# Kernel optimization log

Hardware: AMD Instinct MI355X
Metric: run time of the kernel (lower is better)

Reference implementation:

```python
import jax, jax.numpy as jnp
import numpy as np

B, C, O, H, W, K = 8, 64, 64, 96, 96, 3
PAD = 1


def setup_inputs() -> dict:
    key = jax.random.key(0)
    ks = jax.random.split(key, 5)
    x = jax.random.normal(ks[0], (B, C, H, W), jnp.float32)
    # small offset weights so sampled offsets stay O(1) pixel, like a trained net
    offset_w = jax.random.normal(ks[1], (2 * K * K, C, K, K), jnp.float32) * 0.01
    offset_b = jnp.zeros((2 * K * K,), jnp.float32)
    conv_w = jax.random.normal(ks[2], (O, C, K, K), jnp.float32) * (1.0 / np.sqrt(C * K * K))
    conv_b = jax.random.normal(ks[3], (O,), jnp.float32) * 0.01
    return {"x": x, "offset_w": offset_w, "offset_b": offset_b,
            "conv_w": conv_w, "conv_b": conv_b}


def _conv2d(x, w, b, pad):
    out = jax.lax.conv_general_dilated(
        x, w, window_strides=(1, 1), padding=[(pad, pad), (pad, pad)],
        dimension_numbers=("NCHW", "OIHW", "NCHW"))
    return out + b[None, :, None, None]


def _gather(x_flat, yi, xi):
    # x_flat: [B, C, H*W]; yi, xi: [B, K2, H, W] int32 sample indices
    valid = (yi >= 0) & (yi < H) & (xi >= 0) & (xi < W)
    idx = jnp.clip(yi, 0, H - 1) * W + jnp.clip(xi, 0, W - 1)
    idx_f = idx.reshape(idx.shape[0], -1)  # [B, K2*H*W]
    vals = jax.vmap(lambda xf, i: xf[:, i])(x_flat, idx_f)  # [B, C, K2*H*W]
    vals = vals.reshape(x_flat.shape[0], x_flat.shape[1], *idx.shape[1:])
    return vals * valid[:, None].astype(vals.dtype)  # zero padding outside


def _deform_conv2d(x, offset, w, b, pad):
    # Faithful to torchvision.ops.deform_conv2d (v1, 1 offset group, stride 1)
    K2 = K * K
    off = offset.reshape(offset.shape[0], K2, 2, H, W)
    dy, dx = off[:, :, 0], off[:, :, 1]  # (dy, dx) per kernel tap, torchvision order
    ky = jnp.repeat(jnp.arange(K), K).astype(x.dtype)  # row index i of tap k=i*K+j
    kx = jnp.tile(jnp.arange(K), K).astype(x.dtype)    # col index j
    # fractional sample positions [B, K2, H, W]
    py = jnp.arange(H, dtype=x.dtype)[None, None, :, None] - pad + ky[None, :, None, None] + dy
    px = jnp.arange(W, dtype=x.dtype)[None, None, None, :] - pad + kx[None, :, None, None] + dx
    y0 = jnp.floor(py)
    x0 = jnp.floor(px)
    wy = (py - y0)[:, None]  # broadcast over channels
    wx = (px - x0)[:, None]
    y0i = y0.astype(jnp.int32)
    x0i = x0.astype(jnp.int32)
    x_flat = x.reshape(x.shape[0], x.shape[1], H * W)
    g00 = _gather(x_flat, y0i, x0i)
    g01 = _gather(x_flat, y0i, x0i + 1)
    g10 = _gather(x_flat, y0i + 1, x0i)
    g11 = _gather(x_flat, y0i + 1, x0i + 1)
    # bilinear interp -> sampled patches [B, C, K2, H, W]
    sampled = (g00 * (1 - wy) * (1 - wx) + g01 * (1 - wy) * wx
               + g10 * wy * (1 - wx) + g11 * wy * wx)
    out = jnp.einsum("bckhw,ock->bohw", sampled, w.reshape(w.shape[0], w.shape[1], K2))
    return out + b[None, :, None, None]


def reference(x, offset_w, offset_b, conv_w, conv_b):
    offset = _conv2d(x, offset_w, offset_b, PAD)  # [B, 18, H, W]
    return _deform_conv2d(x, offset, conv_w, conv_b, PAD)
```

## Files before the change

kernel.cpp:

```cpp
#include <hip/hip_runtime.h>

#define Bb 8
#define Cc 64
#define Oo 64
#define Hh 96
#define Ww 96
#define HW 9216
#define NOFF 18

typedef __bf16 bf16_t;
typedef __bf16 bf16x2 __attribute__((ext_vector_type(2)));
typedef __bf16 bf16x8 __attribute__((ext_vector_type(8)));
typedef float  f32x4  __attribute__((ext_vector_type(4)));

#define XT_SZ   (Bb*HW*Cc)
#define WTPD_SZ (18*4*64*8)
#define WTPO_SZ (18*2*64*8)

__global__ void xpose_prep(const float* __restrict__ x, const float* __restrict__ cw,
                           const float* __restrict__ ow, bf16_t* __restrict__ xt,
                           bf16_t* __restrict__ wtpd, bf16_t* __restrict__ wtpo) {
    __shared__ float tile[64][65];
    int bid = blockIdx.x;
    if (bid < 1152) {
        int b    = bid / 144;
        int t0   = (bid % 144) * 64;
        int lane = threadIdx.x & 63;
        int sub  = threadIdx.x >> 6;
        const float* xb = x + (size_t)b * Cc * HW;
        #pragma unroll
        for (int i = 0; i < 16; ++i) {
            int c = sub * 16 + i;
            tile[c][lane] = xb[c * HW + t0 + lane];
        }
        __syncthreads();
        bf16_t* xtb = xt + ((size_t)b * HW + t0) * Cc;
        int half = lane >> 5, cpair = lane & 31;
        #pragma unroll
        for (int i = 0; i < 8; ++i) {
            int hw = sub * 16 + half * 8 + i;
            bf16x2 v;
            v[0] = (bf16_t)tile[cpair * 2][hw];
            v[1] = (bf16_t)tile[cpair * 2 + 1][hw];
            *(bf16x2*)&xtb[hw * Cc + cpair * 2] = v;
        }
    } else if (bid < 1170) {
        int n = (bid - 1152) * 256 + threadIdx.x;
        int t = n >> 8; int rem = n & 255; int mt = rem >> 6; int l = rem & 63;
        int o = mt * 16 + (l & 15);
        int kbase = t * 32 + ((l >> 4) & 3) * 8;
        bf16x8 v;
        #pragma unroll
        for (int j = 0; j < 8; ++j) {
            int kidx = kbase + j; int k = kidx >> 6; int c = kidx & 63;
            v[j] = (bf16_t)cw[(o * 64 + c) * 9 + k];
        }
        *(bf16x8*)&wtpd[n * 8] = v;
    } else {
        int n = (bid - 1170) * 256 + threadIdx.x;
        int t = n >> 7; int rem = n & 127; int mt = rem >> 6; int l = rem & 63;
        int oc = mt * 16 + (l & 15);
        int kbase = t * 32 + ((l >> 4) & 3) * 8;
        bf16x8 v;
        #pragma unroll
        for (int j = 0; j < 8; ++j) {
            int kidx = kbase + j; int k = kidx >> 6; int c = kidx & 63;
            v[j] = (oc < NOFF) ? (bf16_t)ow[(oc * 64 + c) * 9 + k] : (bf16_t)0.f;
        }
        *(bf16x8*)&wtpo[n * 8] = v;
    }
}

__global__ __launch_bounds__(256, 3) void fused_dcn(const bf16_t* __restrict__ xt,
        const bf16_t* __restrict__ wtpo, const bf16_t* __restrict__ wtpd,
        const float* __restrict__ ob, const float* __restrict__ cb,
        float* __restrict__ out) {
    __shared__ float offbuf[64 * 20];
    __shared__ bf16_t Sa[4][16 * 72];
    __shared__ bf16_t slab[16 * 16 * Cc];

    int bid = blockIdx.x;
    int b = bid & 7;
    int t8 = bid >> 3;
    int h0 = (t8 / 12) * 8, w0 = (t8 % 12) * 8;
    int tid = threadIdx.x, lane = tid & 63, q = tid >> 6;
    int cg = lane & 7, prow = lane >> 3;
    int cb8 = cg * 8;
    bf16_t* myS = &Sa[q][0];
    int bbase = b * HW;

    int wy0 = min(max(h0 - 4, 0), Hh - 16);
    int wx0 = min(max(w0 - 4, 0), Ww - 16);

    {
        bf16x8 st[8];
        #pragma unroll
        for (int i = 0; i < 8; ++i) {
            int seg = q * 8 + i;
            int row = seg >> 1, half = seg & 1;
            const bf16_t* src = xt + (size_t)(bbase + (wy0 + row) * Ww + wx0) * Cc
                              + half * 512 + lane * 8;
            st[i] = *(const bf16x8*)src;
        }
        #pragma unroll
        for (int i = 0; i < 8; ++i) {
            int seg = q * 8 + i;
            *(bf16x8*)&slab[seg * 512 + lane * 8] = st[i];
        }
    }

    int pl[2], ph[2], pw[2];
    #pragma unroll
    for (int i = 0; i < 2; ++i) {
        pl[i] = q * 16 + i * 8 + prow;
        ph[i] = h0 + q * 2 + i;
        pw[i] = w0 + prow;
    }

    const bf16x8* wtpo_v = (const bf16x8*)wtpo;
    const bf16x8* wtpd_v = (const bf16x8*)wtpd;

    {
        f32x4 acc[2];
        #pragma unroll
        for (int mt = 0; mt < 2; ++mt)
            #pragma unroll
            for (int r = 0; r < 4; ++r) {
                int oc = mt * 16 + ((lane >> 4) & 3) * 4 + r;
                acc[mt][r] = (oc < NOFF) ? ob[oc] : 0.f;
            }
        bf16x8 g[2];
        bf16x8 wreg[2][2][2];
        auto issue = [&](int k, bf16x8 (&gg)[2]) {
            const int ky = k / 3, kx = k % 3;
            #pragma unroll
            for (int i = 0; i < 2; ++i) {
                int y = ph[i] - 1 + ky, x = pw[i] - 1 + kx;
                bool valid = (y >= 0) && (y < Hh) && (x >= 0) && (x < Ww);
                bf16x8 v;
                #pragma unroll
                for (int j = 0; j < 8; ++j) v[j] = (bf16_t)0.f;
                if (valid)
                    v = *(const bf16x8*)&slab[((y - wy0) * 16 + (x - wx0)) * Cc + cb8];
                gg[i] = v;
            }
        };
        auto loadw = [&](int k, bf16x8 (&w)[2][2]) {
            #pragma unroll
            for (int s = 0; s < 2; ++s)
                #pragma unroll
                for (int mt = 0; mt < 2; ++mt)
                    w[s][mt] = wtpo_v[((k * 2 + s) * 2 + mt) * 64 + lane];
        };
        loadw(0, wreg[0]);
        __syncthreads();
        issue(0, g);
        #pragma unroll
        for (int k = 0; k < 9; ++k) {
            #pragma unroll
            for (int i = 0; i < 2; ++i)
                *(bf16x8*)&myS[(i * 8 + prow) * 72 + cb8] = g[i];
            if (k < 8) { issue(k + 1, g); loadw(k + 1, wreg[(k + 1) & 1]); }
            #pragma unroll
            for (int s = 0; s < 2; ++s) {
                bf16x8 bfrag = *(bf16x8*)&myS[(lane & 15) * 72 + s * 32 + ((lane >> 4) & 3) * 8];
                #pragma unroll
                for (int mt = 0; mt < 2; ++mt)
                    acc[mt] = __builtin_amdgcn_mfma_f32_16x16x32_bf16(wreg[k & 1][s][mt], bfrag, acc[mt], 0, 0, 0);
            }
        }
        #pragma unroll
        for (int mt = 0; mt < 2; ++mt)
            #pragma unroll
            for (int r = 0; r < 4; ++r) {
                int oc = mt * 16 + ((lane >> 4) & 3) * 4 + r;
                if (oc < NOFF)
                    offbuf[(q * 16 + (lane & 15)) * 20 + oc] = acc[mt][r];
            }
    }

    f32x4 acc[4];
    #pragma unroll
    for (int mt = 0; mt < 4; ++mt)
        #pragma unroll
        for (int r = 0; r < 4; ++r)
            acc[mt][r] = cb[mt * 16 + ((lane >> 4) & 3) * 4 + r];

    bf16x8 g[2][4];
    float w4[2][4];
    bf16x8 wreg[2][2][4];
    auto issue = [&](int k, bf16x8 (&gg)[2][4], float (&ww)[2][4]) {
        const int ky = k / 3, kx = k % 3;
        #pragma unroll
        for (int i = 0; i < 2; ++i) {
            float2 od = *(float2*)&offbuf[pl[i] * 20 + 2 * k];
            float py = (float)(ph[i] - 1 + ky) + od.x;
            float px = (float)(pw[i] - 1 + kx) + od.y;
            float fy = floorf(py), fx = floorf(px);
            float wy = py - fy, wx = px - fx;
            int y0 = (int)fy, x0 = (int)fx;
            int y1 = y0 + 1, x1 = x0 + 1;
            bool vy0 = (unsigned)y0 < (unsigned)Hh, vy1 = (unsigned)y1 < (unsigned)Hh;
            bool vx0 = (unsigned)x0 < (unsigned)Ww, vx1 = (unsigned)x1 < (unsigned)Ww;
            ww[i][0] = (vy0 && vx0) ? (1.f - wy) * (1.f - wx) : 0.f;
            ww[i][1] = (vy0 && vx1) ? (1.f - wy) * wx : 0.f;
            ww[i][2] = (vy1 && vx0) ? wy * (1.f - wx) : 0.f;
            ww[i][3] = (vy1 && vx1) ? wy * wx : 0.f;
            int sy0 = min(max(y0 - wy0, 0), 15), sy1 = min(max(y1 - wy0, 0), 15);
            int sx0 = min(max(x0 - wx0, 0), 15), sx1 = min(max(x1 - wx0, 0), 15);
            const bf16_t* r0 = &slab[sy0 * (16 * Cc) + cb8];
            const bf16_t* r1 = &slab[sy1 * (16 * Cc) + cb8];
            gg[i][0] = *(const bf16x8*)(r0 + sx0 * Cc);
            gg[i][1] = *(const bf16x8*)(r0 + sx1 * Cc);
            gg[i][2] = *(const bf16x8*)(r1 + sx0 * Cc);
            gg[i][3] = *(const bf16x8*)(r1 + sx1 * Cc);
        }
    };
    auto loadw = [&](int k, bf16x8 (&w)[2][4]) {
        #pragma unroll
        for (int s = 0; s < 2; ++s)
            #pragma unroll
            for (int mt = 0; mt < 4; ++mt)
                w[s][mt] = wtpd_v[((k * 2 + s) * 4 + mt) * 64 + lane];
    };
    issue(0, g, w4);
    loadw(0, wreg[0]);
    #pragma unroll
    for (int k = 0; k < 9; ++k) {
        #pragma unroll
        for (int i = 0; i < 2; ++i) {
            bf16x8 v;
            #pragma unroll
            for (int j = 0; j < 8; ++j) {
                float s = (float)g[i][0][j] * w4[i][0] + (float)g[i][1][j] * w4[i][1]
                        + (float)g[i][2][j] * w4[i][2] + (float)g[i][3][j] * w4[i][3];
                v[j] = (bf16_t)s;
            }
            *(bf16x8*)&myS[(i * 8 + prow) * 72 + cb8] = v;
        }
        if (k < 8) { issue(k + 1, g, w4); loadw(k + 1, wreg[(k + 1) & 1]); }
        #pragma unroll
        for (int s = 0; s < 2; ++s) {
            bf16x8 bfrag = *(bf16x8*)&myS[(lane & 15) * 72 + s * 32 + ((lane >> 4) & 3) * 8];
            #pragma unroll
            for (int mt = 0; mt < 4; ++mt)
                acc[mt] = __builtin_amdgcn_mfma_f32_16x16x32_bf16(wreg[k & 1][s][mt], bfrag, acc[mt], 0, 0, 0);
        }
    }
    #pragma unroll
    for (int mt = 0; mt < 4; ++mt)
        #pragma unroll
        for (int r = 0; r < 4; ++r) {
            int o = mt * 16 + ((lane >> 4) & 3) * 4 + r;
            int pix = q * 16 + (lane & 15);
            out[(b * Oo + o) * HW + (h0 + (pix >> 3)) * Ww + w0 + (pix & 7)] = acc[mt][r];
        }
}

extern "C" void kernel_launch(void* const* d_in, const int* in_sizes, int n_in,
                              void* d_out, int out_size, void* d_ws, size_t ws_size,
                              hipStream_t stream) {
    const float* x  = (const float*)d_in[0];
    const float* ow = (const float*)d_in[1];
    const float* ob = (const float*)d_in[2];
    const float* cw = (const float*)d_in[3];
    const float* cb = (const float*)d_in[4];
    float* out = (float*)d_out;

    bf16_t* xt   = (bf16_t*)d_ws;
    bf16_t* wtpd = xt + XT_SZ;
    bf16_t* wtpo = wtpd + WTPD_SZ;

    xpose_prep<<<1179, 256, 0, stream>>>(x, cw, ow, xt, wtpd, wtpo);
    fused_dcn <<<1152, 256, 0, stream>>>(xt, wtpo, wtpd, ob, cb, out);
}
```

Baseline: 107.1 us.

## Apply bilinear weights after MFMA on raw corner samples read directly from swizzled slab

The deform stage no longer blends four corners into a bf16 tile per tap. It now runs separate MFMAs on each of the four raw corner samples, read straight from an XOR-swizzled LDS slab, and scales the fp32 results by per-pixel bilinear weights. This drops the per-warp staging buffer, the LDS write/read round trip and the fp32 blend ALU work, and avoids the extra bf16 rounding of the blended value. In exchange it does four times as many MFMAs in the deform stage and adds scalar FMA accumulation, and it removes the software prefetch of weights and samples. The prep kernel's block-to-batch mapping is also interleaved.

```diff
diff --git a/kernel.cpp b/kernel.cpp
--- a/kernel.cpp
+++ b/kernel.cpp
@@ -23,8 +23,8 @@
     __shared__ float tile[64][65];
     int bid = blockIdx.x;
     if (bid < 1152) {
-        int b    = bid / 144;
-        int t0   = (bid % 144) * 64;
+        int b    = bid & 7;
+        int t0   = (bid >> 3) * 64;
         int lane = threadIdx.x & 63;
         int sub  = threadIdx.x >> 6;
         const float* xb = x + (size_t)b * Cc * HW;
@@ -76,7 +76,6 @@
         const float* __restrict__ ob, const float* __restrict__ cb,
         float* __restrict__ out) {
     __shared__ float offbuf[64 * 20];
-    __shared__ bf16_t Sa[4][16 * 72];
     __shared__ bf16_t slab[16 * 16 * Cc];
 
     int bid = blockIdx.x;
@@ -84,9 +83,6 @@
     int t8 = bid >> 3;
     int h0 = (t8 / 12) * 8, w0 = (t8 % 12) * 8;
     int tid = threadIdx.x, lane = tid & 63, q = tid >> 6;
-    int cg = lane & 7, prow = lane >> 3;
-    int cb8 = cg * 8;
-    bf16_t* myS = &Sa[q][0];
     int bbase = b * HW;
 
     int wy0 = min(max(h0 - 4, 0), Hh - 16);
@@ -102,157 +98,132 @@
                               + half * 512 + lane * 8;
             st[i] = *(const bf16x8*)src;
         }
-        #pragma unroll
-        for (int i = 0; i < 8; ++i) {
-            int seg = q * 8 + i;
-            *(bf16x8*)&slab[seg * 512 + lane * 8] = st[i];
-        }
-    }
-
-    int pl[2], ph[2], pw[2];
-    #pragma unroll
-    for (int i = 0; i < 2; ++i) {
-        pl[i] = q * 16 + i * 8 + prow;
-        ph[i] = h0 + q * 2 + i;
-        pw[i] = w0 + prow;
-    }
+        int swz = ((lane >> 3) << 6) + (((lane & 7) ^ ((lane >> 3) & 7)) << 3);
+        #pragma unroll
+        for (int i = 0; i < 8; ++i)
+            *(bf16x8*)&slab[(q * 8 + i) * 512 + swz] = st[i];
+    }
+
+    int g4 = (lane >> 4) & 3;
+    int p  = lane & 15;
+    int py_i = h0 + q * 2 + (p >> 3);
+    int px_i = w0 + (p & 7);
 
     const bf16x8* wtpo_v = (const bf16x8*)wtpo;
     const bf16x8* wtpd_v = (const bf16x8*)wtpd;
 
+    bf16x8 bz;
+    #pragma unroll
+    for (int j = 0; j < 8; ++j) bz[j] = (bf16_t)0.f;
+
+    __syncthreads();
+
     {
         f32x4 acc[2];
         #pragma unroll
         for (int mt = 0; mt < 2; ++mt)
             #pragma unroll
             for (int r = 0; r < 4; ++r) {
-                int oc = mt * 16 + ((lane >> 4) & 3) * 4 + r;
+                int oc = mt * 16 + g4 * 4 + r;
                 acc[mt][r] = (oc < NOFF) ? ob[oc] : 0.f;
             }
-        bf16x8 g[2];
-        bf16x8 wreg[2][2][2];
-        auto issue = [&](int k, bf16x8 (&gg)[2]) {
+        #pragma unroll
+        for (int k = 0; k < 9; ++k) {
             const int ky = k / 3, kx = k % 3;
-            #pragma unroll
-            for (int i = 0; i < 2; ++i) {
-                int y = ph[i] - 1 + ky, x = pw[i] - 1 + kx;
-                bool valid = (y >= 0) && (y < Hh) && (x >= 0) && (x < Ww);
-                bf16x8 v;
+            int y = py_i - 1 + ky, x = px_i - 1 + kx;
+            bool valid = ((unsigned)y < (unsigned)Hh) && ((unsigned)x < (unsigned)Ww);
+            int pl = (y - wy0) * 16 + (x - wx0);
+            pl = min(max(pl, 0), 255);
+            int idx0 = pl * 64 + ((g4 ^ (pl & 7)) << 3);
+            bf16x8 b0 = *(const bf16x8*)&slab[idx0];
+            bf16x8 b1 = *(const bf16x8*)&slab[idx0 ^ 32];
+            if (!valid) { b0 = bz; b1 = bz; }
+            #pragma unroll
+            for (int mt = 0; mt < 2; ++mt) {
+                bf16x8 w0f = wtpo_v[((k * 2 + 0) * 2 + mt) * 64 + lane];
+                acc[mt] = __builtin_amdgcn_mfma_f32_16x16x32_bf16(w0f, b0, acc[mt], 0, 0, 0);
+            }
+            #pragma unroll
+            for (int mt = 0; mt < 2; ++mt) {
+                bf16x8 w1f = wtpo_v[((k * 2 + 1) * 2 + mt) * 64 + lane];
+                acc[mt] = __builtin_amdgcn_mfma_f32_16x16x32_bf16(w1f, b1, acc[mt], 0, 0, 0);
+            }
+        }
+        #pragma unroll
+        for (int mt = 0; mt < 2; ++mt)
+            #pragma unroll
+            for (int r = 0; r < 4; ++r) {
+                int oc = mt * 16 + g4 * 4 + r;
+                if (oc < NOFF)
+                    offbuf[(q * 16 + p) * 20 + oc] = acc[mt][r];
+            }
+    }
+
+    f32x4 acc[4];
+    #pragma unroll
+    for (int mt = 0; mt < 4; ++mt)
+        #pragma unroll
+        for (int r = 0; r < 4; ++r)
+            acc[mt][r] = cb[mt * 16 + g4 * 4 + r];
+
+    const f32x4 z = {0.f, 0.f, 0.f, 0.f};
+    float fyb = (float)(py_i - 1);
+    float fxb = (float)(px_i - 1);
+
+    #pragma unroll
+    for (int k = 0; k < 9; ++k) {
+        const int ky = k / 3, kx = k % 3;
+        float2 od = *(float2*)&offbuf[(q * 16 + p) * 20 + 2 * k];
+        float py = fyb + (float)ky + od.x;
+        float px = fxb + (float)kx + od.y;
+        float fy = floorf(py), fx = floorf(px);
+        float wy = py - fy, wx = px - fx;
+        int y0 = (int)fy, x0 = (int)fx;
+        int y1 = y0 + 1, x1 = x0 + 1;
+        bool vy0 = (unsigned)y0 < (unsigned)Hh, vy1 = (unsigned)y1 < (unsigned)Hh;
+        bool vx0 = (unsigned)x0 < (unsigned)Ww, vx1 = (unsigned)x1 < (unsigned)Ww;
+        float wy1 = 1.f - wy, wx1 = 1.f - wx;
+        float wc[4];
+        wc[0] = (vy0 && vx0) ? wy1 * wx1 : 0.f;
+        wc[1] = (vy0 && vx1) ? wy1 * wx  : 0.f;
+        wc[2] = (vy1 && vx0) ? wy  * wx1 : 0.f;
+        wc[3] = (vy1 && vx1) ? wy  * wx  : 0.f;
+        int pl00 = (y0 - wy0) * 16 + (x0 - wx0);
+        int pls[4];
+        pls[0] = min(max(pl00,      0), 255);
+        pls[1] = min(max(pl00 +  1, 0), 255);
+        pls[2] = min(max(pl00 + 16, 0), 255);
+        pls[3] = min(max(pl00 + 17, 0), 255);
+
+        bf16x8 wf[2][4];
+        #pragma unroll
+        for (int s = 0; s < 2; ++s)
+            #pragma unroll
+            for (int mt = 0; mt < 4; ++mt)
+                wf[s][mt] = wtpd_v[((k * 2 + s) * 4 + mt) * 64 + lane];
+
+        #pragma unroll
+        for (int c = 0; c < 4; ++c) {
+            int idx0 = pls[c] * 64 + ((g4 ^ (pls[c] & 7)) << 3);
+            bf16x8 b0 = *(const bf16x8*)&slab[idx0];
+            bf16x8 b1 = *(const bf16x8*)&slab[idx0 ^ 32];
+            #pragma unroll
+            for (int mt = 0; mt < 4; ++mt) {
+                f32x4 t = __builtin_amdgcn_mfma_f32_16x16x32_bf16(wf[0][mt], b0, z, 0, 0, 0);
+                t = __builtin_amdgcn_mfma_f32_16x16x32_bf16(wf[1][mt], b1, t, 0, 0, 0);
                 #pragma unroll
-                for (int j = 0; j < 8; ++j) v[j] = (bf16_t)0.f;
-                if (valid)
-                    v = *(const bf16x8*)&slab[((y - wy0) * 16 + (x - wx0)) * Cc + cb8];
-                gg[i] = v;
-            }
-        };
-        auto loadw = [&](int k, bf16x8 (&w)[2][2]) {
-            #pragma unroll
-            for (int s = 0; s < 2; ++s)
-                #pragma unroll
-                for (int mt = 0; mt < 2; ++mt)
-                    w[s][mt] = wtpo_v[((k * 2 + s) * 2 + mt) * 64 + lane];
-        };
-        loadw(0, wreg[0]);
-        __syncthreads();
-        issue(0, g);
-        #pragma unroll
-        for (int k = 0; k < 9; ++k) {
-            #pragma unroll
-            for (int i = 0; i < 2; ++i)
-                *(bf16x8*)&myS[(i * 8 + prow) * 72 + cb8] = g[i];
-            if (k < 8) { issue(k + 1, g); loadw(k + 1, wreg[(k + 1) & 1]); }
-            #pragma unroll
-            for (int s = 0; s < 2; ++s) {
-                bf16x8 bfrag = *(bf16x8*)&myS[(lane & 15) * 72 + s * 32 + ((lane >> 4) & 3) * 8];
-                #pragma unroll
-                for (int mt = 0; mt < 2; ++mt)
-                    acc[mt] = __builtin_amdgcn_mfma_f32_16x16x32_bf16(wreg[k & 1][s][mt], bfrag, acc[mt], 0, 0, 0);
-            }
-        }
-        #pragma unroll
-        for (int mt = 0; mt < 2; ++mt)
-            #pragma unroll
-            for (int r = 0; r < 4; ++r) {
-                int oc = mt * 16 + ((lane >> 4) & 3) * 4 + r;
-                if (oc < NOFF)
-                    offbuf[(q * 16 + (lane & 15)) * 20 + oc] = acc[mt][r];
-            }
-    }
-
-    f32x4 acc[4];
+                for (int r = 0; r < 4; ++r)
+                    acc[mt][r] += wc[c] * t[r];
+            }
+        }
+    }
+
     #pragma unroll
     for (int mt = 0; mt < 4; ++mt)
         #pragma unroll
-        for (int r = 0; r < 4; ++r)
-            acc[mt][r] = cb[mt * 16 + ((lane >> 4) & 3) * 4 + r];
-
-    bf16x8 g[2][4];
-    float w4[2][4];
-    bf16x8 wreg[2][2][4];
-    auto issue = [&](int k, bf16x8 (&gg)[2][4], float (&ww)[2][4]) {
-        const int ky = k / 3, kx = k % 3;
-        #pragma unroll
-        for (int i = 0; i < 2; ++i) {
-            float2 od = *(float2*)&offbuf[pl[i] * 20 + 2 * k];
-            float py = (float)(ph[i] - 1 + ky) + od.x;
-            float px = (float)(pw[i] - 1 + kx) + od.y;
-            float fy = floorf(py), fx = floorf(px);
-            float wy = py - fy, wx = px - fx;
-            int y0 = (int)fy, x0 = (int)fx;
-            int y1 = y0 + 1, x1 = x0 + 1;
-            bool vy0 = (unsigned)y0 < (unsigned)Hh, vy1 = (unsigned)y1 < (unsigned)Hh;
-            bool vx0 = (unsigned)x0 < (unsigned)Ww, vx1 = (unsigned)x1 < (unsigned)Ww;
-            ww[i][0] = (vy0 && vx0) ? (1.f - wy) * (1.f - wx) : 0.f;
-            ww[i][1] = (vy0 && vx1) ? (1.f - wy) * wx : 0.f;
-            ww[i][2] = (vy1 && vx0) ? wy * (1.f - wx) : 0.f;
-            ww[i][3] = (vy1 && vx1) ? wy * wx : 0.f;
-            int sy0 = min(max(y0 - wy0, 0), 15), sy1 = min(max(y1 - wy0, 0), 15);
-            int sx0 = min(max(x0 - wx0, 0), 15), sx1 = min(max(x1 - wx0, 0), 15);
-            const bf16_t* r0 = &slab[sy0 * (16 * Cc) + cb8];
-            const bf16_t* r1 = &slab[sy1 * (16 * Cc) + cb8];
-            gg[i][0] = *(const bf16x8*)(r0 + sx0 * Cc);
-            gg[i][1] = *(const bf16x8*)(r0 + sx1 * Cc);
-            gg[i][2] = *(const bf16x8*)(r1 + sx0 * Cc);
-            gg[i][3] = *(const bf16x8*)(r1 + sx1 * Cc);
-        }
-    };
-    auto loadw = [&](int k, bf16x8 (&w)[2][4]) {
-        #pragma unroll
-        for (int s = 0; s < 2; ++s)
-            #pragma unroll
-            for (int mt = 0; mt < 4; ++mt)
-                w[s][mt] = wtpd_v[((k * 2 + s) * 4 + mt) * 64 + lane];
-    };
-    issue(0, g, w4);
-    loadw(0, wreg[0]);
-    #pragma unroll
-    for (int k = 0; k < 9; ++k) {
-        #pragma unroll
-        for (int i = 0; i < 2; ++i) {
-            bf16x8 v;
-            #pragma unroll
-            for (int j = 0; j < 8; ++j) {
-                float s = (float)g[i][0][j] * w4[i][0] + (float)g[i][1][j] * w4[i][1]
-                        + (float)g[i][2][j] * w4[i][2] + (float)g[i][3][j] * w4[i][3];
-                v[j] = (bf16_t)s;
-            }
-            *(bf16x8*)&myS[(i * 8 + prow) * 72 + cb8] = v;
-        }
-        if (k < 8) { issue(k + 1, g, w4); loadw(k + 1, wreg[(k + 1) & 1]); }
-        #pragma unroll
-        for (int s = 0; s < 2; ++s) {
-            bf16x8 bfrag = *(bf16x8*)&myS[(lane & 15) * 72 + s * 32 + ((lane >> 4) & 3) * 8];
-            #pragma unroll
-            for (int mt = 0; mt < 4; ++mt)
-                acc[mt] = __builtin_amdgcn_mfma_f32_16x16x32_bf16(wreg[k & 1][s][mt], bfrag, acc[mt], 0, 0, 0);
-        }
-    }
-    #pragma unroll
-    for (int mt = 0; mt < 4; ++mt)
-        #pragma unroll
         for (int r = 0; r < 4; ++r) {
-            int o = mt * 16 + ((lane >> 4) & 3) * 4 + r;
-            int pix = q * 16 + (lane & 15);
+            int o = mt * 16 + g4 * 4 + r;
+            int pix = q * 16 + p;
             out[(b * Oo + o) * HW + (h0 + (pix >> 3)) * Ww + w0 + (pix & 7)] = acc[mt][r];
         }
 }
```

Result: no change. 108.0 us (+0.9%).
